# Kernel tuning notes

Measured on AMD Instinct MI355X. Metric: run time of the kernel, lower is better.

## Reference

```python
import jax, jax.numpy as jnp
import numpy as np

B, L, D, H, NBLK, NNBR = 256, 200, 128, 2, 2, 10
ITEMS, USERS = 100001, 50001
NEG = -1e9
EPS = 1e-8


def layernorm(x, s, b):
    mu = jnp.mean(x, axis=-1, keepdims=True)
    var = jnp.mean(jnp.square(x - mu), axis=-1, keepdims=True)
    return (x - mu) / jnp.sqrt(var + EPS) * s + b


def mha(q, kv, Wqkv_i, bqkv_i, Wo_i, bo_i, causal_bias):
    # torch.nn.MultiheadAttention math (eval mode), Q from layernormed seq, K=V=seq
    d = q.shape[-1]
    hd = d // H
    Wq, Wk, Wv = Wqkv_i[:d], Wqkv_i[d:2 * d], Wqkv_i[2 * d:]
    bq, bk, bv = bqkv_i[:d], bqkv_i[d:2 * d], bqkv_i[2 * d:]
    Q = (q @ Wq.T + bq).reshape(q.shape[0], q.shape[1], H, hd)
    K = (kv @ Wk.T + bk).reshape(q.shape[0], q.shape[1], H, hd)
    V = (kv @ Wv.T + bv).reshape(q.shape[0], q.shape[1], H, hd)
    scores = jnp.einsum('bqhd,bkhd->bhqk', Q, K) / jnp.sqrt(jnp.float32(hd))
    attn = jax.nn.softmax(scores + causal_bias, axis=-1)
    out = jnp.einsum('bhqk,bkhd->bqhd', attn, V).reshape(q.shape[0], q.shape[1], d)
    return out @ Wo_i.T + bo_i


def setup_inputs() -> dict:
    key = jax.random.key(0)
    ks = jax.random.split(key, 12)
    s = 0.02
    inp = {
        'log_seqs': jax.random.randint(ks[0], (B, L), 0, ITEMS),
        'nbr_idx': jax.random.randint(ks[1], (B, L, NNBR), 0, USERS),
        'item_emb': jax.random.normal(ks[2], (ITEMS, D), jnp.float32) * s,
        'user_emb': jax.random.normal(ks[3], (USERS, D), jnp.float32) * s,
        'pos_emb': jax.random.normal(ks[4], (L, D), jnp.float32) * s,
        'attn_ln_s': jnp.ones((NBLK, D), jnp.float32),
        'attn_ln_b': jnp.zeros((NBLK, D), jnp.float32),
        'Wqkv': jax.random.normal(ks[5], (NBLK, 3 * D, D), jnp.float32) * s,
        'bqkv': jnp.zeros((NBLK, 3 * D), jnp.float32),
        'Wo': jax.random.normal(ks[6], (NBLK, D, D), jnp.float32) * s,
        'bo': jnp.zeros((NBLK, D), jnp.float32),
        'ffn_ln_s': jnp.ones((NBLK, D), jnp.float32),
        'ffn_ln_b': jnp.zeros((NBLK, D), jnp.float32),
        'W1': jax.random.normal(ks[7], (NBLK, D, D), jnp.float32) * s,
        'b1': jnp.zeros((NBLK, D), jnp.float32),
        'W2': jax.random.normal(ks[8], (NBLK, D, D), jnp.float32) * s,
        'b2': jnp.zeros((NBLK, D), jnp.float32),
        'last_ln_s': jnp.ones((D,), jnp.float32),
        'last_ln_b': jnp.zeros((D,), jnp.float32),
        'iui_ln_s': jnp.ones((D,), jnp.float32),
        'iui_ln_b': jnp.zeros((D,), jnp.float32),
    }
    return inp


def reference(log_seqs, nbr_idx, item_emb, user_emb, pos_emb, attn_ln_s, attn_ln_b,
              Wqkv, bqkv, Wo, bo, ffn_ln_s, ffn_ln_b, W1, b1, W2, b2,
              last_ln_s, last_ln_b, iui_ln_s, iui_ln_b):
    d = item_emb.shape[1]
    seqlen = log_seqs.shape[1]
    # SASRec log2feats core (eval mode, dropout disabled)
    seqs = item_emb[log_seqs] * jnp.sqrt(jnp.float32(d)) + pos_emb[None, :seqlen]
    tl_mask = (log_seqs != 0)[..., None].astype(seqs.dtype)
    seqs = seqs * tl_mask
    causal_bias = jnp.where(jnp.tril(jnp.ones((seqlen, seqlen), bool)), 0.0, NEG)
    for i in range(Wqkv.shape[0]):
        q = layernorm(seqs, attn_ln_s[i], attn_ln_b[i])
        seqs = q + mha(q, seqs, Wqkv[i], bqkv[i], Wo[i], bo[i], causal_bias)
        x = layernorm(seqs, ffn_ln_s[i], ffn_ln_b[i])
        # PointWiseFeedForward: 1x1 conv == linear, residual inside
        h = jax.nn.relu(x @ W1[i].T + b1[i]) @ W2[i].T + b2[i]
        seqs = (h + x) * tl_mask
    feats = layernorm(seqs, last_ln_s, last_ln_b)
    # iui meta-path: gather up to 10 user neighbors per item, masked attention aggregation
    qn = item_emb[log_seqs]                       # [B,L,D]
    kn = user_emb[nbr_idx]                        # [B,L,N,D]
    sc = jnp.einsum('bld,blnd->bln', qn, kn) / jnp.sqrt(jnp.float32(d))
    sc = jnp.where(nbr_idx != 0, sc, NEG)
    w = jax.nn.softmax(sc, axis=-1)
    agg = jnp.einsum('bln,blnd->bld', w, kn)
    nbr = layernorm(agg + qn, iui_ln_s, iui_ln_b)
    return feats + nbr
```

## Files before the change

### kernel.cpp

```cpp
#include <hip/hip_runtime.h>
#include <hip/hip_bf16.h>

#define L_SEQ 200
#define DIM 128
#define NROWS (256*200)

typedef __attribute__((ext_vector_type(8))) short bf16x8;
typedef __attribute__((ext_vector_type(4))) float f32x4;

__device__ __forceinline__ float wave_sum(float v){
  #pragma unroll
  for (int o = 32; o; o >>= 1) v += __shfl_xor(v, o);
  return v;
}
__device__ __forceinline__ short f2bf(float f){
  union { float f; unsigned u; } x; x.f = f;
  unsigned r = x.u + 0x7fffu + ((x.u >> 16) & 1u);
  return (short)(r >> 16);
}
__device__ __forceinline__ float bf2f(unsigned short u){
  union { unsigned u; float f; } x; x.u = ((unsigned)u) << 16;
  return x.f;
}

__global__ void cvt_all_kernel(const float* __restrict__ Wqkv, const float* __restrict__ Wo,
                               const float* __restrict__ W1, const float* __restrict__ W2,
                               short* __restrict__ dst){
  int i = blockIdx.x*256 + threadIdx.x;
  if (i >= 49152) return;
  const float* src; int off;
  if (i < 24576)      { src = Wqkv; off = i; }
  else if (i < 32768) { src = Wo;   off = i - 24576; }
  else if (i < 40960) { src = W1;   off = i - 32768; }
  else                { src = W2;   off = i - 40960; }
  float4 v = ((const float4*)src)[off];
  short4 s; s.x = f2bf(v.x); s.y = f2bf(v.y); s.z = f2bf(v.z); s.w = f2bf(v.w);
  ((short4*)dst)[i] = s;
}

__global__ void cvt4_kernel(const float* __restrict__ src, short* __restrict__ dst, int n4){
  int i = blockIdx.x*256 + threadIdx.x;
  if (i < n4) {
    float4 v = ((const float4*)src)[i];
    short4 s; s.x = f2bf(v.x); s.y = f2bf(v.y); s.z = f2bf(v.z); s.w = f2bf(v.w);
    ((short4*)dst)[i] = s;
  }
}

__global__ __launch_bounds__(256) void embed_ln_kernel(
    const int* __restrict__ lsq, const float* __restrict__ item,
    const float* __restrict__ pos, const float* __restrict__ s, const float* __restrict__ b,
    short* __restrict__ seqs_b, short* __restrict__ lnq_b, short* __restrict__ qn_b){
  int wave = threadIdx.x >> 6, lane = threadIdx.x & 63;
  size_t r = (size_t)blockIdx.x*4 + wave;
  int it = lsq[r];
  float2 iv = ((const float2*)(item + (size_t)it*DIM))[lane];
  float2 p = ((const float2*)(pos + (r % L_SEQ)*DIM))[lane];
  short2 qv; qv.x = f2bf(iv.x); qv.y = f2bf(iv.y);
  ((short2*)(qn_b + r*DIM))[lane] = qv;
  float vx = 0.f, vy = 0.f;
  if (it) {
    vx = iv.x * 11.313708498984761f + p.x;
    vy = iv.y * 11.313708498984761f + p.y;
  }
  short2 sv; sv.x = f2bf(vx); sv.y = f2bf(vy);
  ((short2*)(seqs_b + r*DIM))[lane] = sv;
  float mu = wave_sum(vx + vy) * (1.f/DIM);
  float dx = vx - mu, dy = vy - mu;
  float var = wave_sum(dx*dx + dy*dy) * (1.f/DIM);
  float inv = 1.f / sqrtf(var + 1e-8f);
  float2 sc = ((const float2*)s)[lane];
  float2 bc = ((const float2*)b)[lane];
  short2 ov; ov.x = f2bf(dx*inv*sc.x + bc.x); ov.y = f2bf(dy*inv*sc.y + bc.y);
  ((short2*)(lnq_b + r*DIM))[lane] = ov;
}

#define MLP_MFMA(accv) do { \
  _Pragma("unroll") \
  for (int kc = 0; kc < 4; ++kc) { \
    bf16x8 af[4], bfr[2]; \
    _Pragma("unroll") \
    for (int mf = 0; mf < 4; ++mf) { \
      int rr = mbase + mf*16 + col; \
      int byt = (rr*256 + kc*64 + g*16) ^ ((rr & 7) << 4); \
      af[mf] = *(bf16x8*)(AsB + byt); \
    } \
    _Pragma("unroll") \
    for (int nf = 0; nf < 2; ++nf) { \
      int rr = nbase + nf*16 + col; \
      int byt = (rr*256 + kc*64 + g*16) ^ ((rr & 7) << 4); \
      bfr[nf] = *(bf16x8*)(BsB + byt); \
    } \
    _Pragma("unroll") \
    for (int mf = 0; mf < 4; ++mf) \
      _Pragma("unroll") \
      for (int nf = 0; nf < 2; ++nf) \
        accv[mf][nf] = __builtin_amdgcn_mfma_f32_16x16x32_bf16(af[mf], bfr[nf], accv[mf][nf], 0, 0, 0); \
  } \
} while(0)

#define LN_REDUCE(accv) do { \
  _Pragma("unroll") \
  for (int mf = 0; mf < 4; ++mf) { \
    _Pragma("unroll") \
    for (int r = 0; r < 4; ++r) { \
      float s1 = accv[mf][0][r] + accv[mf][1][r]; \
      float s2 = accv[mf][0][r]*accv[mf][0][r] + accv[mf][1][r]*accv[mf][1][r]; \
      _Pragma("unroll") \
      for (int o = 1; o <= 8; o <<= 1) { s1 += __shfl_xor(s1, o); s2 += __shfl_xor(s2, o); } \
      if (col == 0) { int rL = mbase + mf*16 + g*4 + r; redP[0][wn][rL] = s1; redP[1][wn][rL] = s2; } \
    } \
  } \
  __syncthreads(); \
  if (t < 128) { \
    float s1 = redP[0][0][t] + redP[0][1][t] + redP[0][2][t] + redP[0][3][t]; \
    float s2 = redP[1][0][t] + redP[1][1][t] + redP[1][2][t] + redP[1][3][t]; \
    float mu_ = s1 * (1.f/DIM); \
    float var_ = s2 * (1.f/DIM) - mu_*mu_; \
    muA[t] = mu_; invA[t] = 1.f / sqrtf(var_ + 1e-8f); \
  } \
  __syncthreads(); \
} while(0)

__global__ __launch_bounds__(512) void qkv_kernel(
    const short* __restrict__ lnq, const short* __restrict__ seqs,
    const short* __restrict__ Wb, const float* __restrict__ bias,
    short* __restrict__ C){
  __shared__ short As[16384];
  __shared__ short Bs[16384];
  char* AsB = (char*)As; char* BsB = (char*)Bs;
  const int row0 = blockIdx.y * 128, col0 = blockIdx.x * 128;
  const int t = threadIdx.x;
  const short* Ap = (blockIdx.x == 0) ? lnq : seqs;

  #pragma unroll
  for (int i = 0; i < 4; ++i) {
    int flat = t*8 + i*4096;
    int rr = flat >> 7, cc = flat & 127;
    bf16x8 a8 = *(const bf16x8*)(Ap + (size_t)(row0 + rr)*128 + cc);
    int byt = (rr*256 + cc*2) ^ ((rr & 7) << 4);
    *(bf16x8*)(AsB + byt) = a8;
    bf16x8 b8 = *(const bf16x8*)(Wb + (size_t)(col0 + rr)*128 + cc);
    *(bf16x8*)(BsB + byt) = b8;
  }
  __syncthreads();

  const int w = t >> 6, l = t & 63;
  const int wm = w >> 2, wn = w & 3;
  const int col = l & 15, g = l >> 4;
  const int mbase = wm*64, nbase = wn*32;

  f32x4 acc[4][2];
  #pragma unroll
  for (int mf = 0; mf < 4; ++mf)
    #pragma unroll
    for (int nf = 0; nf < 2; ++nf) { f32x4 z = {0.f,0.f,0.f,0.f}; acc[mf][nf] = z; }
  MLP_MFMA(acc);

  float biasv[2];
  #pragma unroll
  for (int nf = 0; nf < 2; ++nf) biasv[nf] = bias[col0 + nbase + nf*16 + col];
  const float qs = (blockIdx.x == 0) ? 0.125f : 1.f;
  #pragma unroll
  for (int mf = 0; mf < 4; ++mf)
    #pragma unroll
    for (int r = 0; r < 4; ++r) {
      int rr = row0 + mbase + mf*16 + g*4 + r;
      #pragma unroll
      for (int nf = 0; nf < 2; ++nf) {
        int cc = col0 + nbase + nf*16 + col;
        float v = (acc[mf][nf][r] + biasv[nf]) * qs;
        C[(size_t)rr*384 + cc] = f2bf(v);
      }
    }
}

template<int WRITE_C>
__global__ __launch_bounds__(512) void mlp_kernel(
    const short* __restrict__ qkvQ, const short* __restrict__ resq,
    const short* __restrict__ wo_b, const float* __restrict__ bo,
    const float* __restrict__ ffnS, const float* __restrict__ ffnB,
    const short* __restrict__ w1_b, const float* __restrict__ b1,
    const short* __restrict__ w2_b, const float* __restrict__ b2,
    const int* __restrict__ lsq,
    short* __restrict__ C,
    const float* __restrict__ lnS2, const float* __restrict__ lnB2,
    short* __restrict__ lnOut){
  __shared__ short As[16384];
  __shared__ short Bs[16384];
  __shared__ float redP[2][4][128];
  __shared__ float muA[128], invA[128];
  char* AsB = (char*)As; char* BsB = (char*)Bs;
  const int row0 = blockIdx.x * 128;
  const int t = threadIdx.x;

  #pragma unroll
  for (int i = 0; i < 4; ++i) {
    int flat = t*8 + i*4096;
    int rr = flat >> 7, cc = flat & 127;
    bf16x8 a8 = *(const bf16x8*)(qkvQ + (size_t)(row0 + rr)*384 + cc);
    int byt = (rr*256 + cc*2) ^ ((rr & 7) << 4);
    *(bf16x8*)(AsB + byt) = a8;
    bf16x8 b8 = *(const bf16x8*)(wo_b + (size_t)rr*128 + cc);
    *(bf16x8*)(BsB + byt) = b8;
  }
  __syncthreads();

  const int w = t >> 6, l = t & 63;
  const int wm = w >> 2, wn = w & 3;
  const int col = l & 15, g = l >> 4;
  const int mbase = wm*64, nbase = wn*32;

  f32x4 acc[4][2];
  #pragma unroll
  for (int mf = 0; mf < 4; ++mf)
    #pragma unroll
    for (int nf = 0; nf < 2; ++nf) { f32x4 z = {0.f,0.f,0.f,0.f}; acc[mf][nf] = z; }
  MLP_MFMA(acc);

  float bov[2];
  #pragma unroll
  for (int nf = 0; nf < 2; ++nf) bov[nf] = bo[nbase + nf*16 + col];
  #pragma unroll
  for (int mf = 0; mf < 4; ++mf)
    #pragma unroll
    for (int r = 0; r < 4; ++r) {
      int rL = mbase + mf*16 + g*4 + r;
      #pragma unroll
      for (int nf = 0; nf < 2; ++nf) {
        int cL = nbase + nf*16 + col;
        acc[mf][nf][r] += bov[nf] + bf2f(((const unsigned short*)resq)[(size_t)(row0 + rL)*DIM + cL]);
      }
    }
  LN_REDUCE(acc);

  float xv[4][2][4];
  #pragma unroll
  for (int mf = 0; mf < 4; ++mf)
    #pragma unroll
    for (int r = 0; r < 4; ++r) {
      int rL = mbase + mf*16 + g*4 + r;
      float mu = muA[rL], inv = invA[rL];
      #pragma unroll
      for (int nf = 0; nf < 2; ++nf) {
        int cL = nbase + nf*16 + col;
        float lnv = (acc[mf][nf][r] - mu)*inv*ffnS[cL] + ffnB[cL];
        xv[mf][nf][r] = lnv;
        int byt = (rL*256 + cL*2) ^ ((rL & 7) << 4);
        *(short*)(AsB + byt) = f2bf(lnv);
      }
    }
  #pragma unroll
  for (int i = 0; i < 4; ++i) {
    int flat = t*8 + i*4096;
    int rr = flat >> 7, cc = flat & 127;
    bf16x8 b8 = *(const bf16x8*)(w1_b + (size_t)rr*128 + cc);
    int byt = (rr*256 + cc*2) ^ ((rr & 7) << 4);
    *(bf16x8*)(BsB + byt) = b8;
  }
  __syncthreads();

  #pragma unroll
  for (int mf = 0; mf < 4; ++mf)
    #pragma unroll
    for (int nf = 0; nf < 2; ++nf) { f32x4 z = {0.f,0.f,0.f,0.f}; acc[mf][nf] = z; }
  MLP_MFMA(acc);
  __syncthreads();

  float b1v[2];
  #pragma unroll
  for (int nf = 0; nf < 2; ++nf) b1v[nf] = b1[nbase + nf*16 + col];
  #pragma unroll
  for (int mf = 0; mf < 4; ++mf)
    #pragma unroll
    for (int r = 0; r < 4; ++r) {
      int rL = mbase + mf*16 + g*4 + r;
      #pragma unroll
      for (int nf = 0; nf < 2; ++nf) {
        int cL = nbase + nf*16 + col;
        float h = fmaxf(acc[mf][nf][r] + b1v[nf], 0.f);
        int byt = (rL*256 + cL*2) ^ ((rL & 7) << 4);
        *(short*)(AsB + byt) = f2bf(h);
      }
    }
  #pragma unroll
  for (int i = 0; i < 4; ++i) {
    int flat = t*8 + i*4096;
    int rr = flat >> 7, cc = flat & 127;
    bf16x8 b8 = *(const bf16x8*)(w2_b + (size_t)rr*128 + cc);
    int byt = (rr*256 + cc*2) ^ ((rr & 7) << 4);
    *(bf16x8*)(BsB + byt) = b8;
  }
  __syncthreads();

  #pragma unroll
  for (int mf = 0; mf < 4; ++mf)
    #pragma unroll
    for (int nf = 0; nf < 2; ++nf) { f32x4 z = {0.f,0.f,0.f,0.f}; acc[mf][nf] = z; }
  MLP_MFMA(acc);

  float b2v[2];
  #pragma unroll
  for (int nf = 0; nf < 2; ++nf) b2v[nf] = b2[nbase + nf*16 + col];
  #pragma unroll
  for (int mf = 0; mf < 4; ++mf)
    #pragma unroll
    for (int r = 0; r < 4; ++r) {
      int rL = mbase + mf*16 + g*4 + r;
      bool zr = (lsq[row0 + rL] == 0);
      #pragma unroll
      for (int nf = 0; nf < 2; ++nf) {
        float v = acc[mf][nf][r] + b2v[nf] + xv[mf][nf][r];
        if (zr) v = 0.f;
        acc[mf][nf][r] = v;
      }
    }
  LN_REDUCE(acc);
  #pragma unroll
  for (int mf = 0; mf < 4; ++mf)
    #pragma unroll
    for (int r = 0; r < 4; ++r) {
      int rL = mbase + mf*16 + g*4 + r;
      float mu = muA[rL], inv = invA[rL];
      #pragma unroll
      for (int nf = 0; nf < 2; ++nf) {
        int cL = nbase + nf*16 + col;
        float v = acc[mf][nf][r];
        float lnv = (v - mu)*inv*lnS2[cL] + lnB2[cL];
        lnOut[(size_t)(row0 + rL)*DIM + cL] = f2bf(lnv);
        if (WRITE_C) C[(size_t)(row0 + rL)*DIM + cL] = f2bf(v);
      }
    }
}

__global__ __launch_bounds__(512) void attn_kernel(short* __restrict__ qkv){
  __shared__ short Ks[224*64];
  __shared__ short Vt[64*224];
  __shared__ short Ps[8][16*232];
  const int b = blockIdx.x >> 1, h = blockIdx.x & 1;
  short* base = qkv + (size_t)b*L_SEQ*384 + h*64;
  const short* baseK = base + 128;
  const short* baseV = base + 256;
  const int t = threadIdx.x;
  char* KsB = (char*)Ks;
  char* VtB = (char*)Vt;

  for (int idx = t; idx < 224*8; idx += 512) {
    int row = idx >> 3, c8 = idx & 7;
    bf16x8 kv = {0,0,0,0,0,0,0,0}, vv = {0,0,0,0,0,0,0,0};
    if (row < L_SEQ) {
      kv = *(const bf16x8*)(baseK + (size_t)row*384 + c8*8);
      vv = *(const bf16x8*)(baseV + (size_t)row*384 + c8*8);
    }
    int kbyte = (row*128 + c8*16) ^ ((row & 7) << 4);
    *(bf16x8*)(KsB + kbyte) = kv;
    #pragma unroll
    for (int e = 0; e < 8; ++e) {
      int d = c8*8 + e;
      int vbyte = (d*448 + row*2) ^ ((d & 7) << 4);
      *(short*)(VtB + vbyte) = vv[e];
    }
  }
  __syncthreads();

  const int w = t >> 6, l = t & 63;
  const int col = l & 15, g = l >> 4, g4 = g * 4;
  char* PB = (char*)Ps[w];

  const int ntiles = (w < 5) ? 2 : 1;
  for (int j = 0; j < ntiles; ++j) {
    const int qt = (j == 0) ? w : 12 - w;
    bf16x8 qf[2];
    {
      int gr = qt*16 + col;
      #pragma unroll
      for (int c = 0; c < 2; ++c) {
        bf16x8 q = {0,0,0,0,0,0,0,0};
        if (gr < L_SEQ) q = *(const bf16x8*)(base + (size_t)gr*384 + c*32 + g*8);
        qf[c] = q;
      }
    }
    f32x4 sc[13];
    #pragma unroll
    for (int kt = 0; kt < 13; ++kt) {
      if (kt <= qt) {
        f32x4 a = {0.f,0.f,0.f,0.f};
        #pragma unroll
        for (int c = 0; c < 2; ++c) {
          int row = kt*16 + col;
          int byt = (row*128 + c*64 + g*16) ^ ((row & 7) << 4);
          bf16x8 kf = *(bf16x8*)(KsB + byt);
          a = __builtin_amdgcn_mfma_f32_16x16x32_bf16(qf[c], kf, a, 0, 0, 0);
        }
        sc[kt] = a;
      }
    }
    float m[4] = {-1e30f,-1e30f,-1e30f,-1e30f};
    #pragma unroll
    for (int kt = 0; kt < 13; ++kt) {
      if (kt <= qt) {
        #pragma unroll
        for (int r = 0; r < 4; ++r) {
          bool ok = (kt < qt) || (col <= g4 + r);
          if (!ok) sc[kt][r] = -1e30f;
          m[r] = fmaxf(m[r], sc[kt][r]);
        }
      }
    }
    #pragma unroll
    for (int r = 0; r < 4; ++r) {
      #pragma unroll
      for (int o = 1; o <= 8; o <<= 1) m[r] = fmaxf(m[r], __shfl_xor(m[r], o));
    }
    float s[4] = {0.f,0.f,0.f,0.f};
    #pragma unroll
    for (int kt = 0; kt < 13; ++kt) {
      if (kt <= qt) {
        #pragma unroll
        for (int r = 0; r < 4; ++r) {
          float e = __expf(sc[kt][r] - m[r]);
          sc[kt][r] = e;
          s[r] += e;
        }
      }
    }
    float inv[4];
    #pragma unroll
    for (int r = 0; r < 4; ++r) {
      #pragma unroll
      for (int o = 1; o <= 8; o <<= 1) s[r] += __shfl_xor(s[r], o);
      inv[r] = 1.f / s[r];
    }
    #pragma unroll
    for (int kt = 0; kt < 13; ++kt) {
      if (kt <= qt) {
        #pragma unroll
        for (int r = 0; r < 4; ++r)
          *(short*)(PB + ((g4 + r)*232 + kt*16 + col)*2) = f2bf(sc[kt][r]);
      } else if (kt == qt + 1) {
        #pragma unroll
        for (int r = 0; r < 4; ++r)
          *(short*)(PB + ((g4 + r)*232 + kt*16 + col)*2) = 0;
      }
    }
    #pragma unroll
    for (int r = 0; r < 4; ++r)
      *(short*)(PB + ((g4 + r)*232 + 208 + col)*2) = 0;
    asm volatile("s_waitcnt lgkmcnt(0)" ::: "memory");
    f32x4 o4[4];
    #pragma unroll
    for (int nt = 0; nt < 4; ++nt) { f32x4 z = {0.f,0.f,0.f,0.f}; o4[nt] = z; }
    const int kcmax = (qt*16 + 15) >> 5;
    #pragma unroll
    for (int kc = 0; kc < 7; ++kc) {
      if (kc <= kcmax) {
        bf16x8 pf = *(bf16x8*)(PB + col*464 + kc*64 + g*16);
        #pragma unroll
        for (int nt = 0; nt < 4; ++nt) {
          int d = nt*16 + col;
          int byt = (d*448 + kc*64 + g*16) ^ ((d & 7) << 4);
          bf16x8 vf = *(bf16x8*)(VtB + byt);
          o4[nt] = __builtin_amdgcn_mfma_f32_16x16x32_bf16(pf, vf, o4[nt], 0, 0, 0);
        }
      }
    }
    #pragma unroll
    for (int nt = 0; nt < 4; ++nt)
      #pragma unroll
      for (int r = 0; r < 4; ++r) {
        int qr = qt*16 + g4 + r;
        if (qr < L_SEQ) base[(size_t)qr*384 + nt*16 + col] = f2bf(o4[nt][r] * inv[r]);
      }
  }
}

__global__ __launch_bounds__(256) void final_kernel(
    const short* __restrict__ feats_b, const short* __restrict__ qn_b,
    const int* __restrict__ nbr, const short* __restrict__ user_b,
    const float* __restrict__ is_, const float* __restrict__ ib,
    float* __restrict__ out){
  int wave = threadIdx.x >> 6, lane = threadIdx.x & 63;
  int half = lane >> 5, sl = lane & 31;
  size_t r = (size_t)blockIdx.x*8 + wave*2 + half;

  ushort4 fv = ((const ushort4*)(feats_b + r*DIM))[sl];
  float f0 = bf2f(fv.x), f1 = bf2f(fv.y), f2 = bf2f(fv.z), f3 = bf2f(fv.w);
  ushort4 qv4 = ((const ushort4*)(qn_b + r*DIM))[sl];
  float q0 = bf2f(qv4.x), q1 = bf2f(qv4.y), q2 = bf2f(qv4.z), q3 = bf2f(qv4.w);

  int idxs[10];
  #pragma unroll
  for (int n = 0; n < 10; ++n) idxs[n] = nbr[r*10 + n];
  float kn[10][4]; float scn[10];
  #pragma unroll
  for (int n = 0; n < 10; ++n) {
    ushort4 kv = ((const ushort4*)(user_b + (size_t)idxs[n]*DIM))[sl];
    kn[n][0] = bf2f(kv.x); kn[n][1] = bf2f(kv.y); kn[n][2] = bf2f(kv.z); kn[n][3] = bf2f(kv.w);
    float p = q0*kn[n][0] + q1*kn[n][1] + q2*kn[n][2] + q3*kn[n][3];
    #pragma unroll
    for (int o = 1; o <= 16; o <<= 1) p += __shfl_xor(p, o);
    scn[n] = idxs[n] ? p * 0.08838834764831845f : -1.0e9f;
  }
  float m = scn[0];
  #pragma unroll
  for (int n = 1; n < 10; ++n) m = fmaxf(m, scn[n]);
  float w[10], sum = 0.f;
  #pragma unroll
  for (int n = 0; n < 10; ++n) { w[n] = expf(scn[n] - m); sum += w[n]; }
  float invs = 1.f / sum;
  float a0 = 0.f, a1 = 0.f, a2 = 0.f, a3 = 0.f;
  #pragma unroll
  for (int n = 0; n < 10; ++n) {
    a0 += w[n]*kn[n][0]; a1 += w[n]*kn[n][1]; a2 += w[n]*kn[n][2]; a3 += w[n]*kn[n][3];
  }
  a0 = a0*invs + q0;
  a1 = a1*invs + q1;
  a2 = a2*invs + q2;
  a3 = a3*invs + q3;
  float s1 = a0 + a1 + a2 + a3;
  #pragma unroll
  for (int o = 1; o <= 16; o <<= 1) s1 += __shfl_xor(s1, o);
  float mu2 = s1 * (1.f/DIM);
  float d0 = a0 - mu2, d1 = a1 - mu2, d2 = a2 - mu2, d3 = a3 - mu2;
  float sq = d0*d0 + d1*d1 + d2*d2 + d3*d3;
  #pragma unroll
  for (int o = 1; o <= 16; o <<= 1) sq += __shfl_xor(sq, o);
  float inv2 = 1.f / sqrtf(sq * (1.f/DIM) + 1e-8f);
  float4 isc = ((const float4*)is_)[sl], ibc = ((const float4*)ib)[sl];
  float4 o;
  o.x = f0 + d0*inv2*isc.x + ibc.x;
  o.y = f1 + d1*inv2*isc.y + ibc.y;
  o.z = f2 + d2*inv2*isc.z + ibc.z;
  o.w = f3 + d3*inv2*isc.w + ibc.w;
  ((float4*)(out + r*DIM))[sl] = o;
}

extern "C" void kernel_launch(void* const* d_in, const int* in_sizes, int n_in,
                              void* d_out, int out_size, void* d_ws, size_t ws_size,
                              hipStream_t stream) {
  const int*   lsq    = (const int*)d_in[0];
  const int*   nbr    = (const int*)d_in[1];
  const float* item   = (const float*)d_in[2];
  const float* user   = (const float*)d_in[3];
  const float* pos    = (const float*)d_in[4];
  const float* attn_s = (const float*)d_in[5];
  const float* attn_b = (const float*)d_in[6];
  const float* Wqkv   = (const float*)d_in[7];
  const float* bqkv   = (const float*)d_in[8];
  const float* Wo     = (const float*)d_in[9];
  const float* bo     = (const float*)d_in[10];
  const float* ffn_s  = (const float*)d_in[11];
  const float* ffn_b  = (const float*)d_in[12];
  const float* W1     = (const float*)d_in[13];
  const float* b1     = (const float*)d_in[14];
  const float* W2     = (const float*)d_in[15];
  const float* b2     = (const float*)d_in[16];
  const float* last_s = (const float*)d_in[17];
  const float* last_b = (const float*)d_in[18];
  const float* iui_s  = (const float*)d_in[19];
  const float* iui_b  = (const float*)d_in[20];
  float* out = (float*)d_out;

  const int N = NROWS;
  short* seqs_b = (short*)d_ws;
  short* lnq_b  = seqs_b + (size_t)N*DIM;
  short* qkv_b  = lnq_b  + (size_t)N*DIM;
  short* wqkv_b = qkv_b  + (size_t)N*384;
  short* wo_b   = wqkv_b + 2*384*128;
  short* w1_b   = wo_b   + 2*128*128;
  short* w2_b   = w1_b   + 2*128*128;
  short* user_b = w2_b   + 2*128*128;
  short* qn_b   = user_b + (size_t)50001*DIM + 64;

  cvt_all_kernel<<<192, 256, 0, stream>>>(Wqkv, Wo, W1, W2, wqkv_b);
  cvt4_kernel<<<(50001*DIM/4 + 255)/256, 256, 0, stream>>>(user, user_b, 50001*DIM/4);

  embed_ln_kernel<<<N/4, 256, 0, stream>>>(lsq, item, pos, attn_s, attn_b,
                                           seqs_b, lnq_b, qn_b);

  for (int i = 0; i < 2; ++i) {
    qkv_kernel<<<dim3(3, N/128), 512, 0, stream>>>(
        lnq_b, seqs_b, wqkv_b + (size_t)i*384*128, bqkv + i*384, qkv_b);
    attn_kernel<<<256*2, 512, 0, stream>>>(qkv_b);
    if (i == 0) {
      mlp_kernel<1><<<N/128, 512, 0, stream>>>(
          qkv_b, lnq_b, wo_b, bo, ffn_s, ffn_b,
          w1_b, b1, w2_b, b2, lsq,
          seqs_b, attn_s + DIM, attn_b + DIM, lnq_b);
    } else {
      mlp_kernel<0><<<N/128, 512, 0, stream>>>(
          qkv_b, lnq_b, wo_b + 128*128, bo + DIM, ffn_s + DIM, ffn_b + DIM,
          w1_b + 128*128, b1 + DIM, w2_b + 128*128, b2 + DIM, lsq,
          nullptr, last_s, last_b, lnq_b);
    }
  }

  final_kernel<<<N/8, 256, 0, stream>>>(lnq_b, qn_b, nbr, user_b,
                                        iui_s, iui_b, out);
}
```

Measured before the change: 211.0 us.

## Fuse QKV projection into attention kernel, computing K/V/Q per batch-head in LDS

The separate QKV GEMM kernel is removed. Each attention block now projects K and V for its batch-head straight into shared memory, and projects Q per query tile into the per-wave P buffer. This removes the write and re-read of the N×384 qkv buffer in global memory and one kernel launch per block. In exchange, weights are loaded from global or L2 directly into registers by every block, and the projection work is repeated per head-block rather than batched. Register pressure also rises from holding the weight fragments.

```diff
diff --git a/kernel.cpp b/kernel.cpp
--- a/kernel.cpp
+++ b/kernel.cpp
@@ -122,62 +122,239 @@
   __syncthreads(); \
 } while(0)
 
-__global__ __launch_bounds__(512) void qkv_kernel(
+__global__ __launch_bounds__(512) void fattn_kernel(
     const short* __restrict__ lnq, const short* __restrict__ seqs,
     const short* __restrict__ Wb, const float* __restrict__ bias,
-    short* __restrict__ C){
-  __shared__ short As[16384];
-  __shared__ short Bs[16384];
-  char* AsB = (char*)As; char* BsB = (char*)Bs;
-  const int row0 = blockIdx.y * 128, col0 = blockIdx.x * 128;
+    short* __restrict__ ao){
+  __shared__ short Ks[224*64];
+  __shared__ short Vt[64*224];
+  __shared__ short Ps[8][16*232];
+  const int b = blockIdx.x >> 1, h = blockIdx.x & 1;
   const int t = threadIdx.x;
-  const short* Ap = (blockIdx.x == 0) ? lnq : seqs;
-
-  #pragma unroll
-  for (int i = 0; i < 4; ++i) {
-    int flat = t*8 + i*4096;
-    int rr = flat >> 7, cc = flat & 127;
-    bf16x8 a8 = *(const bf16x8*)(Ap + (size_t)(row0 + rr)*128 + cc);
-    int byt = (rr*256 + cc*2) ^ ((rr & 7) << 4);
-    *(bf16x8*)(AsB + byt) = a8;
-    bf16x8 b8 = *(const bf16x8*)(Wb + (size_t)(col0 + rr)*128 + cc);
-    *(bf16x8*)(BsB + byt) = b8;
+  char* KsB = (char*)Ks; char* VtB = (char*)Vt;
+  const int w = t >> 6, l = t & 63;
+  const int col = l & 15, g = l >> 4, g4 = g * 4;
+  char* PB = (char*)Ps[w];
+  const int ntiles = (w < 5) ? 2 : 1;
+  const size_t rowbase = (size_t)b * L_SEQ;
+
+  bf16x8 av[2][4];
+  #pragma unroll
+  for (int j = 0; j < 2; ++j) {
+    int mt = (j == 0) ? w : 12 - w;
+    int sr = mt*16 + col;
+    bool vld = (j < ntiles) && (sr < L_SEQ);
+    #pragma unroll
+    for (int kc = 0; kc < 4; ++kc) {
+      bf16x8 z = {0,0,0,0,0,0,0,0};
+      av[j][kc] = vld ? *(const bf16x8*)(seqs + (rowbase + sr)*DIM + kc*32 + g*8) : z;
+    }
+  }
+  {
+    bf16x8 wk[4][4]; float bk[4];
+    #pragma unroll
+    for (int nf = 0; nf < 4; ++nf) {
+      int jj = nf*16 + col;
+      bk[nf] = bias[128 + h*64 + jj];
+      #pragma unroll
+      for (int kc = 0; kc < 4; ++kc)
+        wk[nf][kc] = *(const bf16x8*)(Wb + (size_t)(128 + h*64 + jj)*DIM + kc*32 + g*8);
+    }
+    #pragma unroll
+    for (int j = 0; j < 2; ++j) {
+      f32x4 ac[4];
+      #pragma unroll
+      for (int nf = 0; nf < 4; ++nf) { f32x4 z = {0.f,0.f,0.f,0.f}; ac[nf] = z; }
+      #pragma unroll
+      for (int kc = 0; kc < 4; ++kc)
+        #pragma unroll
+        for (int nf = 0; nf < 4; ++nf)
+          ac[nf] = __builtin_amdgcn_mfma_f32_16x16x32_bf16(av[j][kc], wk[nf][kc], ac[nf], 0, 0, 0);
+      if (j < ntiles) {
+        int mt = (j == 0) ? w : 12 - w;
+        #pragma unroll
+        for (int nf = 0; nf < 4; ++nf)
+          #pragma unroll
+          for (int r = 0; r < 4; ++r) {
+            int srow = mt*16 + g4 + r;
+            int d = nf*16 + col;
+            *(short*)(KsB + ((srow*128 + d*2) ^ ((srow & 7) << 4))) = f2bf(ac[nf][r] + bk[nf]);
+          }
+      }
+    }
+  }
+  {
+    bf16x8 wv[4][4]; float bv[4];
+    #pragma unroll
+    for (int nf = 0; nf < 4; ++nf) {
+      int jj = nf*16 + col;
+      bv[nf] = bias[256 + h*64 + jj];
+      #pragma unroll
+      for (int kc = 0; kc < 4; ++kc)
+        wv[nf][kc] = *(const bf16x8*)(Wb + (size_t)(256 + h*64 + jj)*DIM + kc*32 + g*8);
+    }
+    #pragma unroll
+    for (int j = 0; j < 2; ++j) {
+      f32x4 ac[4];
+      #pragma unroll
+      for (int nf = 0; nf < 4; ++nf) { f32x4 z = {0.f,0.f,0.f,0.f}; ac[nf] = z; }
+      #pragma unroll
+      for (int kc = 0; kc < 4; ++kc)
+        #pragma unroll
+        for (int nf = 0; nf < 4; ++nf)
+          ac[nf] = __builtin_amdgcn_mfma_f32_16x16x32_bf16(av[j][kc], wv[nf][kc], ac[nf], 0, 0, 0);
+      if (j < ntiles) {
+        int mt = (j == 0) ? w : 12 - w;
+        #pragma unroll
+        for (int nf = 0; nf < 4; ++nf)
+          #pragma unroll
+          for (int r = 0; r < 4; ++r) {
+            int srow = mt*16 + g4 + r;
+            int d = nf*16 + col;
+            *(short*)(VtB + ((d*448 + srow*2) ^ ((d & 7) << 4))) = f2bf(ac[nf][r] + bv[nf]);
+          }
+      }
+    }
   }
   __syncthreads();
 
-  const int w = t >> 6, l = t & 63;
-  const int wm = w >> 2, wn = w & 3;
-  const int col = l & 15, g = l >> 4;
-  const int mbase = wm*64, nbase = wn*32;
-
-  f32x4 acc[4][2];
-  #pragma unroll
-  for (int mf = 0; mf < 4; ++mf)
-    #pragma unroll
-    for (int nf = 0; nf < 2; ++nf) { f32x4 z = {0.f,0.f,0.f,0.f}; acc[mf][nf] = z; }
-  MLP_MFMA(acc);
-
-  float biasv[2];
-  #pragma unroll
-  for (int nf = 0; nf < 2; ++nf) biasv[nf] = bias[col0 + nbase + nf*16 + col];
-  const float qs = (blockIdx.x == 0) ? 0.125f : 1.f;
-  #pragma unroll
-  for (int mf = 0; mf < 4; ++mf)
+  for (int j = 0; j < ntiles; ++j) {
+    const int qt = (j == 0) ? w : 12 - w;
+    {
+      bf16x8 qa[4];
+      int sr = qt*16 + col;
+      bool vld = sr < L_SEQ;
+      #pragma unroll
+      for (int kc = 0; kc < 4; ++kc) {
+        bf16x8 z = {0,0,0,0,0,0,0,0};
+        qa[kc] = vld ? *(const bf16x8*)(lnq + (rowbase + sr)*DIM + kc*32 + g*8) : z;
+      }
+      f32x4 aq[4];
+      #pragma unroll
+      for (int nf = 0; nf < 4; ++nf) { f32x4 z = {0.f,0.f,0.f,0.f}; aq[nf] = z; }
+      #pragma unroll
+      for (int kc = 0; kc < 4; ++kc)
+        #pragma unroll
+        for (int nf = 0; nf < 4; ++nf) {
+          bf16x8 wq = *(const bf16x8*)(Wb + (size_t)(h*64 + nf*16 + col)*DIM + kc*32 + g*8);
+          aq[nf] = __builtin_amdgcn_mfma_f32_16x16x32_bf16(qa[kc], wq, aq[nf], 0, 0, 0);
+        }
+      #pragma unroll
+      for (int nf = 0; nf < 4; ++nf) {
+        float bq = bias[h*64 + nf*16 + col];
+        #pragma unroll
+        for (int r = 0; r < 4; ++r) {
+          int srow = g4 + r;
+          int d = nf*16 + col;
+          float v = (aq[nf][r] + bq) * 0.125f;
+          *(short*)(PB + ((srow*128 + d*2) ^ ((srow & 7) << 4))) = f2bf(v);
+        }
+      }
+    }
+    bf16x8 qf[2];
+    #pragma unroll
+    for (int c = 0; c < 2; ++c) {
+      int row = col;
+      qf[c] = *(bf16x8*)(PB + ((row*128 + c*64 + g*16) ^ ((row & 7) << 4)));
+    }
+
+    f32x4 sc[13];
+    #pragma unroll
+    for (int kt = 0; kt < 13; ++kt) {
+      if (kt <= qt) {
+        f32x4 a = {0.f,0.f,0.f,0.f};
+        #pragma unroll
+        for (int c = 0; c < 2; ++c) {
+          int row = kt*16 + col;
+          int byt = (row*128 + c*64 + g*16) ^ ((row & 7) << 4);
+          bf16x8 kf = *(bf16x8*)(KsB + byt);
+          a = __builtin_amdgcn_mfma_f32_16x16x32_bf16(qf[c], kf, a, 0, 0, 0);
+        }
+        sc[kt] = a;
+      }
+    }
+    float m[4] = {-1e30f,-1e30f,-1e30f,-1e30f};
+    #pragma unroll
+    for (int kt = 0; kt < 13; ++kt) {
+      if (kt <= qt) {
+        #pragma unroll
+        for (int r = 0; r < 4; ++r) {
+          bool ok = (kt < qt) || (col <= g4 + r);
+          if (!ok) sc[kt][r] = -1e30f;
+          m[r] = fmaxf(m[r], sc[kt][r]);
+        }
+      }
+    }
     #pragma unroll
     for (int r = 0; r < 4; ++r) {
-      int rr = row0 + mbase + mf*16 + g*4 + r;
-      #pragma unroll
-      for (int nf = 0; nf < 2; ++nf) {
-        int cc = col0 + nbase + nf*16 + col;
-        float v = (acc[mf][nf][r] + biasv[nf]) * qs;
-        C[(size_t)rr*384 + cc] = f2bf(v);
-      }
-    }
+      #pragma unroll
+      for (int o = 1; o <= 8; o <<= 1) m[r] = fmaxf(m[r], __shfl_xor(m[r], o));
+    }
+    float s[4] = {0.f,0.f,0.f,0.f};
+    #pragma unroll
+    for (int kt = 0; kt < 13; ++kt) {
+      if (kt <= qt) {
+        #pragma unroll
+        for (int r = 0; r < 4; ++r) {
+          float e = __expf(sc[kt][r] - m[r]);
+          sc[kt][r] = e;
+          s[r] += e;
+        }
+      }
+    }
+    float inv[4];
+    #pragma unroll
+    for (int r = 0; r < 4; ++r) {
+      #pragma unroll
+      for (int o = 1; o <= 8; o <<= 1) s[r] += __shfl_xor(s[r], o);
+      inv[r] = 1.f / s[r];
+    }
+    #pragma unroll
+    for (int kt = 0; kt < 13; ++kt) {
+      if (kt <= qt) {
+        #pragma unroll
+        for (int r = 0; r < 4; ++r)
+          *(short*)(PB + ((g4 + r)*232 + kt*16 + col)*2) = f2bf(sc[kt][r]);
+      } else if (kt == qt + 1) {
+        #pragma unroll
+        for (int r = 0; r < 4; ++r)
+          *(short*)(PB + ((g4 + r)*232 + kt*16 + col)*2) = 0;
+      }
+    }
+    #pragma unroll
+    for (int r = 0; r < 4; ++r)
+      *(short*)(PB + ((g4 + r)*232 + 208 + col)*2) = 0;
+    asm volatile("s_waitcnt lgkmcnt(0)" ::: "memory");
+    f32x4 o4[4];
+    #pragma unroll
+    for (int nt = 0; nt < 4; ++nt) { f32x4 z = {0.f,0.f,0.f,0.f}; o4[nt] = z; }
+    const int kcmax = (qt*16 + 15) >> 5;
+    #pragma unroll
+    for (int kc = 0; kc < 7; ++kc) {
+      if (kc <= kcmax) {
+        bf16x8 pf = *(bf16x8*)(PB + col*464 + kc*64 + g*16);
+        #pragma unroll
+        for (int nt = 0; nt < 4; ++nt) {
+          int d = nt*16 + col;
+          int byt = (d*448 + kc*64 + g*16) ^ ((d & 7) << 4);
+          bf16x8 vf = *(bf16x8*)(VtB + byt);
+          o4[nt] = __builtin_amdgcn_mfma_f32_16x16x32_bf16(pf, vf, o4[nt], 0, 0, 0);
+        }
+      }
+    }
+    #pragma unroll
+    for (int nt = 0; nt < 4; ++nt)
+      #pragma unroll
+      for (int r = 0; r < 4; ++r) {
+        int qr = qt*16 + g4 + r;
+        if (qr < L_SEQ) ao[(rowbase + qr)*DIM + h*64 + nt*16 + col] = f2bf(o4[nt][r] * inv[r]);
+      }
+  }
 }
 
 template<int WRITE_C>
 __global__ __launch_bounds__(512) void mlp_kernel(
-    const short* __restrict__ qkvQ, const short* __restrict__ resq,
+    const short* __restrict__ aoQ, const short* __restrict__ resq,
     const short* __restrict__ wo_b, const float* __restrict__ bo,
     const float* __restrict__ ffnS, const float* __restrict__ ffnB,
     const short* __restrict__ w1_b, const float* __restrict__ b1,
@@ -198,7 +375,7 @@
   for (int i = 0; i < 4; ++i) {
     int flat = t*8 + i*4096;
     int rr = flat >> 7, cc = flat & 127;
-    bf16x8 a8 = *(const bf16x8*)(qkvQ + (size_t)(row0 + rr)*384 + cc);
+    bf16x8 a8 = *(const bf16x8*)(aoQ + (size_t)(row0 + rr)*DIM + cc);
     int byt = (rr*256 + cc*2) ^ ((rr & 7) << 4);
     *(bf16x8*)(AsB + byt) = a8;
     bf16x8 b8 = *(const bf16x8*)(wo_b + (size_t)rr*128 + cc);
@@ -331,147 +508,6 @@
         if (WRITE_C) C[(size_t)(row0 + rL)*DIM + cL] = f2bf(v);
       }
     }
-}
-
-__global__ __launch_bounds__(512) void attn_kernel(short* __restrict__ qkv){
-  __shared__ short Ks[224*64];
-  __shared__ short Vt[64*224];
-  __shared__ short Ps[8][16*232];
-  const int b = blockIdx.x >> 1, h = blockIdx.x & 1;
-  short* base = qkv + (size_t)b*L_SEQ*384 + h*64;
-  const short* baseK = base + 128;
-  const short* baseV = base + 256;
-  const int t = threadIdx.x;
-  char* KsB = (char*)Ks;
-  char* VtB = (char*)Vt;
-
-  for (int idx = t; idx < 224*8; idx += 512) {
-    int row = idx >> 3, c8 = idx & 7;
-    bf16x8 kv = {0,0,0,0,0,0,0,0}, vv = {0,0,0,0,0,0,0,0};
-    if (row < L_SEQ) {
-      kv = *(const bf16x8*)(baseK + (size_t)row*384 + c8*8);
-      vv = *(const bf16x8*)(baseV + (size_t)row*384 + c8*8);
-    }
-    int kbyte = (row*128 + c8*16) ^ ((row & 7) << 4);
-    *(bf16x8*)(KsB + kbyte) = kv;
-    #pragma unroll
-    for (int e = 0; e < 8; ++e) {
-      int d = c8*8 + e;
-      int vbyte = (d*448 + row*2) ^ ((d & 7) << 4);
-      *(short*)(VtB + vbyte) = vv[e];
-    }
-  }
-  __syncthreads();
-
-  const int w = t >> 6, l = t & 63;
-  const int col = l & 15, g = l >> 4, g4 = g * 4;
-  char* PB = (char*)Ps[w];
-
-  const int ntiles = (w < 5) ? 2 : 1;
-  for (int j = 0; j < ntiles; ++j) {
-    const int qt = (j == 0) ? w : 12 - w;
-    bf16x8 qf[2];
-    {
-      int gr = qt*16 + col;
-      #pragma unroll
-      for (int c = 0; c < 2; ++c) {
-        bf16x8 q = {0,0,0,0,0,0,0,0};
-        if (gr < L_SEQ) q = *(const bf16x8*)(base + (size_t)gr*384 + c*32 + g*8);
-        qf[c] = q;
-      }
-    }
-    f32x4 sc[13];
-    #pragma unroll
-    for (int kt = 0; kt < 13; ++kt) {
-      if (kt <= qt) {
-        f32x4 a = {0.f,0.f,0.f,0.f};
-        #pragma unroll
-        for (int c = 0; c < 2; ++c) {
-          int row = kt*16 + col;
-          int byt = (row*128 + c*64 + g*16) ^ ((row & 7) << 4);
-          bf16x8 kf = *(bf16x8*)(KsB + byt);
-          a = __builtin_amdgcn_mfma_f32_16x16x32_bf16(qf[c], kf, a, 0, 0, 0);
-        }
-        sc[kt] = a;
-      }
-    }
-    float m[4] = {-1e30f,-1e30f,-1e30f,-1e30f};
-    #pragma unroll
-    for (int kt = 0; kt < 13; ++kt) {
-      if (kt <= qt) {
-        #pragma unroll
-        for (int r = 0; r < 4; ++r) {
-          bool ok = (kt < qt) || (col <= g4 + r);
-          if (!ok) sc[kt][r] = -1e30f;
-          m[r] = fmaxf(m[r], sc[kt][r]);
-        }
-      }
-    }
-    #pragma unroll
-    for (int r = 0; r < 4; ++r) {
-      #pragma unroll
-      for (int o = 1; o <= 8; o <<= 1) m[r] = fmaxf(m[r], __shfl_xor(m[r], o));
-    }
-    float s[4] = {0.f,0.f,0.f,0.f};
-    #pragma unroll
-    for (int kt = 0; kt < 13; ++kt) {
-      if (kt <= qt) {
-        #pragma unroll
-        for (int r = 0; r < 4; ++r) {
-          float e = __expf(sc[kt][r] - m[r]);
-          sc[kt][r] = e;
-          s[r] += e;
-        }
-      }
-    }
-    float inv[4];
-    #pragma unroll
-    for (int r = 0; r < 4; ++r) {
-      #pragma unroll
-      for (int o = 1; o <= 8; o <<= 1) s[r] += __shfl_xor(s[r], o);
-      inv[r] = 1.f / s[r];
-    }
-    #pragma unroll
-    for (int kt = 0; kt < 13; ++kt) {
-      if (kt <= qt) {
-        #pragma unroll
-        for (int r = 0; r < 4; ++r)
-          *(short*)(PB + ((g4 + r)*232 + kt*16 + col)*2) = f2bf(sc[kt][r]);
-      } else if (kt == qt + 1) {
-        #pragma unroll
-        for (int r = 0; r < 4; ++r)
-          *(short*)(PB + ((g4 + r)*232 + kt*16 + col)*2) = 0;
-      }
-    }
-    #pragma unroll
-    for (int r = 0; r < 4; ++r)
-      *(short*)(PB + ((g4 + r)*232 + 208 + col)*2) = 0;
-    asm volatile("s_waitcnt lgkmcnt(0)" ::: "memory");
-    f32x4 o4[4];
-    #pragma unroll
-    for (int nt = 0; nt < 4; ++nt) { f32x4 z = {0.f,0.f,0.f,0.f}; o4[nt] = z; }
-    const int kcmax = (qt*16 + 15) >> 5;
-    #pragma unroll
-    for (int kc = 0; kc < 7; ++kc) {
-      if (kc <= kcmax) {
-        bf16x8 pf = *(bf16x8*)(PB + col*464 + kc*64 + g*16);
-        #pragma unroll
-        for (int nt = 0; nt < 4; ++nt) {
-          int d = nt*16 + col;
-          int byt = (d*448 + kc*64 + g*16) ^ ((d & 7) << 4);
-          bf16x8 vf = *(bf16x8*)(VtB + byt);
-          o4[nt] = __builtin_amdgcn_mfma_f32_16x16x32_bf16(pf, vf, o4[nt], 0, 0, 0);
-        }
-      }
-    }
-    #pragma unroll
-    for (int nt = 0; nt < 4; ++nt)
-      #pragma unroll
-      for (int r = 0; r < 4; ++r) {
-        int qr = qt*16 + g4 + r;
-        if (qr < L_SEQ) base[(size_t)qr*384 + nt*16 + col] = f2bf(o4[nt][r] * inv[r]);
-      }
-  }
 }
 
 __global__ __launch_bounds__(256) void final_kernel(
@@ -564,8 +600,8 @@
   const int N = NROWS;
   short* seqs_b = (short*)d_ws;
   short* lnq_b  = seqs_b + (size_t)N*DIM;
-  short* qkv_b  = lnq_b  + (size_t)N*DIM;
-  short* wqkv_b = qkv_b  + (size_t)N*384;
+  short* ao_b   = lnq_b  + (size_t)N*DIM;
+  short* wqkv_b = ao_b   + (size_t)N*DIM;
   short* wo_b   = wqkv_b + 2*384*128;
   short* w1_b   = wo_b   + 2*128*128;
   short* w2_b   = w1_b   + 2*128*128;
@@ -579,17 +615,16 @@
                                            seqs_b, lnq_b, qn_b);
 
   for (int i = 0; i < 2; ++i) {
-    qkv_kernel<<<dim3(3, N/128), 512, 0, stream>>>(
-        lnq_b, seqs_b, wqkv_b + (size_t)i*384*128, bqkv + i*384, qkv_b);
-    attn_kernel<<<256*2, 512, 0, stream>>>(qkv_b);
+    fattn_kernel<<<256*2, 512, 0, stream>>>(
+        lnq_b, seqs_b, wqkv_b + (size_t)i*384*128, bqkv + i*384, ao_b);
     if (i == 0) {
       mlp_kernel<1><<<N/128, 512, 0, stream>>>(
-          qkv_b, lnq_b, wo_b, bo, ffn_s, ffn_b,
+          ao_b, lnq_b, wo_b, bo, ffn_s, ffn_b,
           w1_b, b1, w2_b, b2, lsq,
           seqs_b, attn_s + DIM, attn_b + DIM, lnq_b);
     } else {
       mlp_kernel<0><<<N/128, 512, 0, stream>>>(
-          qkv_b, lnq_b, wo_b + 128*128, bo + DIM, ffn_s + DIM, ffn_b + DIM,
+          ao_b, lnq_b, wo_b + 128*128, bo + DIM, ffn_s + DIM, ffn_b + DIM,
           w1_b + 128*128, b1 + DIM, w2_b + 128*128, b2 + DIM, lsq,
           nullptr, last_s, last_b, lnq_b);
     }
```

New measurement: 276.0 us. 1.31x slower.
